# Kernel tuning notes

Hardware: AMD Instinct MI355X
Metric: run time of the kernel (lower is better)

The kernel has to match this reference:

```python
import jax, jax.numpy as jnp
import numpy as np

N = 10000
E = 320000
F_IN = 256
F_PROJ = 200


def setup_inputs() -> dict:
    key = jax.random.key(0)
    ks = jax.random.split(key, 8)
    x = jax.random.normal(ks[0], (N, F_IN), dtype=jnp.float32)
    edge_attr = jax.random.uniform(ks[1], (N, N), dtype=jnp.float32)
    src = jax.random.randint(ks[2], (E,), 0, N)
    dst = jax.random.randint(ks[3], (E,), 0, N)
    # remove self loops at data-gen time (module calls remove_self_loops)
    dst = jnp.where(dst == src, (dst + 1) % N, dst)
    edge_index = jnp.stack([src, dst]).astype(jnp.int64)
    W_proj = jax.random.normal(ks[4], (F_IN, F_PROJ), dtype=jnp.float32) * 0.05
    b_proj = jnp.zeros((F_PROJ,), dtype=jnp.float32)
    W_att = jax.random.normal(ks[5], (F_PROJ, 1), dtype=jnp.float32) * 0.05
    b_att = jnp.zeros((1,), dtype=jnp.float32)
    return {"x": x, "edge_attr": edge_attr, "edge_index": edge_index,
            "W_proj": W_proj, "b_proj": b_proj, "W_att": W_att, "b_att": b_att}


def reference(x, edge_attr, edge_index, W_proj, b_proj, W_att, b_att):
    src, dst = edge_index[0], edge_index[1]
    # gather: x_j = source features, x_i = target features (PyG default flow)
    x_i = x[dst]                      # [E, F_IN]
    x_j = x[src]                      # [E, F_IN]
    p_i = x_i @ W_proj + b_proj       # [E, 200]
    p_j = x_j @ W_proj + b_proj       # [E, 200]
    alpha = jnp.abs(p_i - p_j) @ W_att + b_att   # [E, 1]
    alpha = jax.nn.relu(alpha)
    alpha = jax.nn.softmax(alpha, axis=0)        # softmax over edges
    a = alpha[:, 0]
    # write attention symmetrically into the dense edge matrix
    edge_values = edge_attr.at[src, dst].set(a).at[dst, src].set(a)
    # scatter-max aggregation of (unprojected) x_i by target index
    agg = jax.ops.segment_max(x_i, dst, num_segments=N)
    agg = jnp.where(jnp.isfinite(agg), agg, jnp.zeros((), agg.dtype))
    return agg, edge_values
```

## Files before the change

kernel.cpp:

```cpp
#include <hip/hip_runtime.h>

#define N_NODES 10000
#define E_EDGES 320000
#define F_IN    256
#define F_PROJ  200

typedef float vfloat4 __attribute__((ext_vector_type(4)));

#define ROW_F4      2500L
#define R1          2400
#define R2          6200
#define C1_F4_BEG   0L
#define C1_F4_END   (R1 * ROW_F4)
#define C2_F4_BEG   C1_F4_END
#define C2_F4_END   ((long)R2 * ROW_F4)
#define C3_F4_BEG   C2_F4_END
#define C3_F4_END   (N_NODES * ROW_F4)

#define PJ_BLOCKS   2500
#define K1_COPY_BLOCKS 1024
#define A_BLOCKS    2048
#define A_CHUNK     40
#define AGG_BLOCKS  160
#define AGG_N4      (N_NODES * F_IN / 4)
#define AGG_PER_BLK (AGG_N4 / AGG_BLOCKS)
#define K2_COPY_BLOCKS 2048
#define K3_COPY_BLOCKS 2048
#define SC_BLOCKS   1250

#define WS_P      0L
#define WS_EXP    4000000L
#define WS_FLAGS  5280000L
#define WS_SUM    5320000L

__device__ __forceinline__ unsigned short f32_to_bf16(float f) {
    unsigned int u = __float_as_uint(f);
    u += 0x7FFFu + ((u >> 16) & 1u);
    return (unsigned short)(u >> 16);
}
__device__ __forceinline__ float bf16_to_f32(unsigned short b) {
    return __uint_as_float(((unsigned int)b) << 16);
}

__device__ __forceinline__ void nt_copy_range(
        const vfloat4* __restrict__ src, vfloat4* __restrict__ dst,
        long beg, long end, int cid, int nblk, int tid) {
    long i = beg + (long)cid * 256 + tid;
    const long stride = (long)nblk * 256;
    for (; i < end; i += stride) {
        vfloat4 v = __builtin_nontemporal_load(src + i);
        __builtin_nontemporal_store(v, dst + i);
    }
}

__global__ __launch_bounds__(256) void k1_proj_flags_copy(
        const float* __restrict__ x, const float* __restrict__ W,
        unsigned short* __restrict__ P, const int* __restrict__ ei,
        int* __restrict__ flags,
        const vfloat4* __restrict__ csrc, vfloat4* __restrict__ cdst) {
    int bid = blockIdx.x, tid = threadIdx.x;
    if (bid >= PJ_BLOCKS) {
        nt_copy_range(csrc, cdst, C1_F4_BEG, C1_F4_END,
                      bid - PJ_BLOCKS, K1_COPY_BLOCKS, tid);
        return;
    }
    int gt = bid * 256 + tid;
    if (gt < E_EDGES) flags[ei[E_EDGES + gt]] = 1;

    __shared__ float xs[4][F_IN];
    int n0 = bid * 4;
    ((float4*)xs)[tid] = ((const float4*)(x + (long)n0 * F_IN))[tid];
    __syncthreads();
    int j = tid;
    if (j >= F_PROJ) return;
    float acc[4] = {0.f, 0.f, 0.f, 0.f};
    for (int k = 0; k < F_IN; ++k) {
        float w = W[k * F_PROJ + j];
        #pragma unroll
        for (int r = 0; r < 4; ++r) acc[r] += xs[r][k] * w;
    }
    #pragma unroll
    for (int r = 0; r < 4; ++r) P[(long)(n0 + r) * F_PROJ + j] = f32_to_bf16(acc[r]);
}

__global__ __launch_bounds__(256) void k2_alpha_agg_copy(
        const int* __restrict__ ei, const unsigned short* __restrict__ P,
        const float* __restrict__ Watt, const float* __restrict__ batt,
        float* __restrict__ expalpha, float* __restrict__ sumbuf,
        const int* __restrict__ flags, const float4* __restrict__ x4,
        float4* __restrict__ agg4,
        const vfloat4* __restrict__ csrc, vfloat4* __restrict__ cdst) {
    int bid = blockIdx.x, tid = threadIdx.x;
    if (bid < A_BLOCKS) {
        __shared__ float bsum;
        if (tid == 0) bsum = 0.f;
        __syncthreads();
        int wid  = bid * 4 + (tid >> 6);
        int lane = tid & 63;
        float4 w4 = make_float4(0.f, 0.f, 0.f, 0.f);
        if (lane < 50) w4 = ((const float4*)Watt)[lane];
        float bias = batt[0];
        int e0 = wid * A_CHUNK;
        int e1 = min(e0 + A_CHUNK, E_EDGES);
        float lsum = 0.f;
        for (int e = e0; e < e1; ++e) {
            int s = ei[e];
            int d = ei[E_EDGES + e];
            float acc = 0.f;
            if (lane < 50) {
                uint2 us = *(const uint2*)(P + (long)s * F_PROJ + lane * 4);
                uint2 ud = *(const uint2*)(P + (long)d * F_PROJ + lane * 4);
                acc = fabsf(bf16_to_f32((unsigned short)(ud.x & 0xFFFF)) -
                            bf16_to_f32((unsigned short)(us.x & 0xFFFF))) * w4.x
                    + fabsf(bf16_to_f32((unsigned short)(ud.x >> 16)) -
                            bf16_to_f32((unsigned short)(us.x >> 16))) * w4.y
                    + fabsf(bf16_to_f32((unsigned short)(ud.y & 0xFFFF)) -
                            bf16_to_f32((unsigned short)(us.y & 0xFFFF))) * w4.z
                    + fabsf(bf16_to_f32((unsigned short)(ud.y >> 16)) -
                            bf16_to_f32((unsigned short)(us.y >> 16))) * w4.w;
            }
            #pragma unroll
            for (int off = 32; off; off >>= 1) acc += __shfl_down(acc, off);
            if (lane == 0) {
                float ea = expf(fmaxf(acc + bias, 0.f));
                expalpha[e] = ea;
                lsum += ea;
            }
        }
        if (lane == 0) atomicAdd(&bsum, lsum);
        __syncthreads();
        if (tid == 0) atomicAdd(sumbuf, bsum);
        return;
    }
    int b2 = bid - A_BLOCKS;
    if (b2 < AGG_BLOCKS) {
        long base = (long)b2 * AGG_PER_BLK;
        for (int i = tid; i < AGG_PER_BLK; i += 256) {
            long i4 = base + i;
            float4 v = x4[i4];
            if (!flags[i4 >> 6]) v = make_float4(0.f, 0.f, 0.f, 0.f);
            agg4[i4] = v;
        }
        return;
    }
    nt_copy_range(csrc, cdst, C2_F4_BEG, C2_F4_END,
                  b2 - AGG_BLOCKS, K2_COPY_BLOCKS, tid);
}

__global__ __launch_bounds__(256) void k3_copy_scatter_lo(
        const int* __restrict__ ei, const float* __restrict__ expalpha,
        const float* __restrict__ sumbuf, float* __restrict__ ev,
        const vfloat4* __restrict__ csrc, vfloat4* __restrict__ cdst) {
    int bid = blockIdx.x, tid = threadIdx.x;
    if (bid < K3_COPY_BLOCKS) {
        nt_copy_range(csrc, cdst, C3_F4_BEG, C3_F4_END, bid, K3_COPY_BLOCKS, tid);
        return;
    }
    int e = (bid - K3_COPY_BLOCKS) * 256 + tid;
    if (e >= E_EDGES) return;
    float a = expalpha[e] / sumbuf[0];
    int s = ei[e], d = ei[E_EDGES + e];
    if (s < R2) ev[(long)s * N_NODES + d] = a;
    if (d < R2) ev[(long)d * N_NODES + s] = a;
}

__global__ __launch_bounds__(256) void k4_scatter_hi(
        const int* __restrict__ ei, const float* __restrict__ expalpha,
        const float* __restrict__ sumbuf, float* __restrict__ ev) {
    int e = blockIdx.x * 256 + threadIdx.x;
    if (e >= E_EDGES) return;
    float a = expalpha[e] / sumbuf[0];
    int s = ei[e], d = ei[E_EDGES + e];
    if (s >= R2) ev[(long)s * N_NODES + d] = a;
    if (d >= R2) ev[(long)d * N_NODES + s] = a;
}

extern "C" void kernel_launch(void* const* d_in, const int* in_sizes, int n_in,
                              void* d_out, int out_size, void* d_ws, size_t ws_size,
                              hipStream_t stream) {
    (void)in_sizes; (void)n_in; (void)out_size; (void)ws_size;
    const float* x         = (const float*)d_in[0];
    const float* edge_attr = (const float*)d_in[1];
    const int*   ei        = (const int*)d_in[2];
    const float* W_proj    = (const float*)d_in[3];
    const float* W_att     = (const float*)d_in[5];
    const float* b_att     = (const float*)d_in[6];

    float* agg = (float*)d_out;
    float* ev  = (float*)d_out + (long)N_NODES * F_IN;
    char* ws = (char*)d_ws;

    unsigned short* P = (unsigned short*)(ws + WS_P);
    float* expalpha   = (float*)(ws + WS_EXP);
    int*   flags      = (int*)(ws + WS_FLAGS);
    float* sumbuf     = (float*)(ws + WS_SUM);

    hipMemsetAsync(ws + WS_FLAGS, 0, 40016, stream);

    k1_proj_flags_copy<<<PJ_BLOCKS + K1_COPY_BLOCKS, 256, 0, stream>>>(
        x, W_proj, P, ei, flags, (const vfloat4*)edge_attr, (vfloat4*)ev);

    k2_alpha_agg_copy<<<A_BLOCKS + AGG_BLOCKS + K2_COPY_BLOCKS, 256, 0, stream>>>(
        ei, P, W_att, b_att, expalpha, sumbuf, flags,
        (const float4*)x, (float4*)agg,
        (const vfloat4*)edge_attr, (vfloat4*)ev);

    k3_copy_scatter_lo<<<K3_COPY_BLOCKS + SC_BLOCKS, 256, 0, stream>>>(
        ei, expalpha, sumbuf, ev, (const vfloat4*)edge_attr, (vfloat4*)ev);

    k4_scatter_hi<<<SC_BLOCKS, 256, 0, stream>>>(ei, expalpha, sumbuf, ev);
}
```

Measured before the change: 253.3 us.

## Prefetch edge_attr halves into cache with touch kernels before flush copies

Splits the 400MB dense copy into two 200MB halves. Each half is first read by a touch pass that runs alongside projection, then copied with a normal load and a nontemporal store, so the copy reads from the last-level cache. This adds an extra full read of edge_attr and one more kernel launch. It relies on a 200MB chunk fitting in the MI355X Infinity Cache (256MB), which is tight and may instead cost extra HBM traffic.

```diff
diff --git a/kernel.cpp b/kernel.cpp
--- a/kernel.cpp
+++ b/kernel.cpp
@@ -7,26 +7,21 @@
 
 typedef float vfloat4 __attribute__((ext_vector_type(4)));
 
-#define ROW_F4      2500L
-#define R1          2400
-#define R2          6200
-#define C1_F4_BEG   0L
-#define C1_F4_END   (R1 * ROW_F4)
-#define C2_F4_BEG   C1_F4_END
-#define C2_F4_END   ((long)R2 * ROW_F4)
-#define C3_F4_BEG   C2_F4_END
-#define C3_F4_END   (N_NODES * ROW_F4)
-
-#define PJ_BLOCKS   2500
-#define K1_COPY_BLOCKS 1024
-#define A_BLOCKS    2048
-#define A_CHUNK     40
-#define AGG_BLOCKS  160
-#define AGG_N4      (N_NODES * F_IN / 4)
-#define AGG_PER_BLK (AGG_N4 / AGG_BLOCKS)
-#define K2_COPY_BLOCKS 2048
-#define K3_COPY_BLOCKS 2048
-#define SC_BLOCKS   1250
+#define ROW_F4     2500L
+#define CHUNK_ROWS 5000L
+#define CHUNK_F4   (CHUNK_ROWS * ROW_F4)
+#define EV_F4      25000000L
+#define RSPLIT     5000
+
+#define PJ_BLOCKS    2500
+#define TOUCH_BLOCKS 2048
+#define FLUSH_BLOCKS 2048
+#define A_BLOCKS     2048
+#define A_CHUNK      40
+#define AGG_BLOCKS   160
+#define AGG_N4       (N_NODES * F_IN / 4)
+#define AGG_PER_BLK  (AGG_N4 / AGG_BLOCKS)
+#define SC_BLOCKS    1250
 
 #define WS_P      0L
 #define WS_EXP    4000000L
@@ -42,26 +37,35 @@
     return __uint_as_float(((unsigned int)b) << 16);
 }
 
-__device__ __forceinline__ void nt_copy_range(
+__device__ __forceinline__ void touch_range(
+        const vfloat4* __restrict__ src, long beg, long end,
+        int cid, int nblk, int tid) {
+    long i = beg + (long)cid * 256 + tid;
+    const long stride = (long)nblk * 256;
+    for (; i < end; i += stride) {
+        vfloat4 v = src[i];
+        asm volatile("" :: "v"(v.x), "v"(v.y), "v"(v.z), "v"(v.w));
+    }
+}
+
+__device__ __forceinline__ void flush_range(
         const vfloat4* __restrict__ src, vfloat4* __restrict__ dst,
         long beg, long end, int cid, int nblk, int tid) {
     long i = beg + (long)cid * 256 + tid;
     const long stride = (long)nblk * 256;
     for (; i < end; i += stride) {
-        vfloat4 v = __builtin_nontemporal_load(src + i);
+        vfloat4 v = src[i];
         __builtin_nontemporal_store(v, dst + i);
     }
 }
 
-__global__ __launch_bounds__(256) void k1_proj_flags_copy(
+__global__ __launch_bounds__(256) void t1_proj_flags_touch(
         const float* __restrict__ x, const float* __restrict__ W,
         unsigned short* __restrict__ P, const int* __restrict__ ei,
-        int* __restrict__ flags,
-        const vfloat4* __restrict__ csrc, vfloat4* __restrict__ cdst) {
+        int* __restrict__ flags, const vfloat4* __restrict__ csrc) {
     int bid = blockIdx.x, tid = threadIdx.x;
     if (bid >= PJ_BLOCKS) {
-        nt_copy_range(csrc, cdst, C1_F4_BEG, C1_F4_END,
-                      bid - PJ_BLOCKS, K1_COPY_BLOCKS, tid);
+        touch_range(csrc, 0L, CHUNK_F4, bid - PJ_BLOCKS, TOUCH_BLOCKS, tid);
         return;
     }
     int gt = bid * 256 + tid;
@@ -83,7 +87,7 @@
     for (int r = 0; r < 4; ++r) P[(long)(n0 + r) * F_PROJ + j] = f32_to_bf16(acc[r]);
 }
 
-__global__ __launch_bounds__(256) void k2_alpha_agg_copy(
+__global__ __launch_bounds__(256) void f1_alpha_agg_flush(
         const int* __restrict__ ei, const unsigned short* __restrict__ P,
         const float* __restrict__ Watt, const float* __restrict__ batt,
         float* __restrict__ expalpha, float* __restrict__ sumbuf,
@@ -143,36 +147,39 @@
         }
         return;
     }
-    nt_copy_range(csrc, cdst, C2_F4_BEG, C2_F4_END,
-                  b2 - AGG_BLOCKS, K2_COPY_BLOCKS, tid);
-}
-
-__global__ __launch_bounds__(256) void k3_copy_scatter_lo(
+    flush_range(csrc, cdst, 0L, CHUNK_F4, b2 - AGG_BLOCKS, FLUSH_BLOCKS, tid);
+}
+
+__global__ __launch_bounds__(256) void t2_touch(const vfloat4* __restrict__ csrc) {
+    touch_range(csrc, CHUNK_F4, EV_F4, blockIdx.x, TOUCH_BLOCKS, threadIdx.x);
+}
+
+__global__ __launch_bounds__(256) void f2_flush_scatter_lo(
         const int* __restrict__ ei, const float* __restrict__ expalpha,
         const float* __restrict__ sumbuf, float* __restrict__ ev,
         const vfloat4* __restrict__ csrc, vfloat4* __restrict__ cdst) {
     int bid = blockIdx.x, tid = threadIdx.x;
-    if (bid < K3_COPY_BLOCKS) {
-        nt_copy_range(csrc, cdst, C3_F4_BEG, C3_F4_END, bid, K3_COPY_BLOCKS, tid);
-        return;
-    }
-    int e = (bid - K3_COPY_BLOCKS) * 256 + tid;
+    if (bid < FLUSH_BLOCKS) {
+        flush_range(csrc, cdst, CHUNK_F4, EV_F4, bid, FLUSH_BLOCKS, tid);
+        return;
+    }
+    int e = (bid - FLUSH_BLOCKS) * 256 + tid;
     if (e >= E_EDGES) return;
     float a = expalpha[e] / sumbuf[0];
     int s = ei[e], d = ei[E_EDGES + e];
-    if (s < R2) ev[(long)s * N_NODES + d] = a;
-    if (d < R2) ev[(long)d * N_NODES + s] = a;
-}
-
-__global__ __launch_bounds__(256) void k4_scatter_hi(
+    if (s < RSPLIT) ev[(long)s * N_NODES + d] = a;
+    if (d < RSPLIT) ev[(long)d * N_NODES + s] = a;
+}
+
+__global__ __launch_bounds__(256) void s_scatter_hi(
         const int* __restrict__ ei, const float* __restrict__ expalpha,
         const float* __restrict__ sumbuf, float* __restrict__ ev) {
     int e = blockIdx.x * 256 + threadIdx.x;
     if (e >= E_EDGES) return;
     float a = expalpha[e] / sumbuf[0];
     int s = ei[e], d = ei[E_EDGES + e];
-    if (s >= R2) ev[(long)s * N_NODES + d] = a;
-    if (d >= R2) ev[(long)d * N_NODES + s] = a;
+    if (s >= RSPLIT) ev[(long)s * N_NODES + d] = a;
+    if (d >= RSPLIT) ev[(long)d * N_NODES + s] = a;
 }
 
 extern "C" void kernel_launch(void* const* d_in, const int* in_sizes, int n_in,
@@ -197,16 +204,18 @@
 
     hipMemsetAsync(ws + WS_FLAGS, 0, 40016, stream);
 
-    k1_proj_flags_copy<<<PJ_BLOCKS + K1_COPY_BLOCKS, 256, 0, stream>>>(
-        x, W_proj, P, ei, flags, (const vfloat4*)edge_attr, (vfloat4*)ev);
-
-    k2_alpha_agg_copy<<<A_BLOCKS + AGG_BLOCKS + K2_COPY_BLOCKS, 256, 0, stream>>>(
+    t1_proj_flags_touch<<<PJ_BLOCKS + TOUCH_BLOCKS, 256, 0, stream>>>(
+        x, W_proj, P, ei, flags, (const vfloat4*)edge_attr);
+
+    f1_alpha_agg_flush<<<A_BLOCKS + AGG_BLOCKS + FLUSH_BLOCKS, 256, 0, stream>>>(
         ei, P, W_att, b_att, expalpha, sumbuf, flags,
         (const float4*)x, (float4*)agg,
         (const vfloat4*)edge_attr, (vfloat4*)ev);
 
-    k3_copy_scatter_lo<<<K3_COPY_BLOCKS + SC_BLOCKS, 256, 0, stream>>>(
+    t2_touch<<<TOUCH_BLOCKS, 256, 0, stream>>>((const vfloat4*)edge_attr);
+
+    f2_flush_scatter_lo<<<FLUSH_BLOCKS + SC_BLOCKS, 256, 0, stream>>>(
         ei, expalpha, sumbuf, ev, (const vfloat4*)edge_attr, (vfloat4*)ev);
 
-    k4_scatter_hi<<<SC_BLOCKS, 256, 0, stream>>>(ei, expalpha, sumbuf, ev);
-}
+    s_scatter_hi<<<SC_BLOCKS, 256, 0, stream>>>(ei, expalpha, sumbuf, ev);
+}
```

New measurement: 315.6 us. +24.6%, slower.
